# Kernel optimization log

Hardware: AMD Instinct MI355X
Metric: run time of the kernel (lower is better)

The kernel has to match this reference:

```python
import jax, jax.numpy as jnp
import numpy as np

E, H, F, N, B = 512, 8, 2048, 1024, 4
HD = E // H


def setup_inputs() -> dict:
    key = jax.random.key(0)
    ks = jax.random.split(key, 20)
    s = 0.02
    return {
        "node_inputs": jax.random.normal(ks[0], (N, B, E), jnp.float32),
        "parent_mask": jax.random.uniform(ks[1], (B, N, N), jnp.float32),
        "hidden": jax.random.bernoulli(ks[2], 0.5, (B, N, N)),
        "pad_mask": jax.random.bernoulli(ks[3], 0.1, (B, N)),
        "Wp": jax.random.normal(ks[4], (H, E), jnp.float32) * s,
        "bp": jnp.zeros((H,), jnp.float32),
        "Wc": jax.random.normal(ks[5], (H, E), jnp.float32) * s,
        "bc": jnp.zeros((H,), jnp.float32),
        "Wqkv": jax.random.normal(ks[6], (3 * E, E), jnp.float32) * s,
        "bqkv": jnp.zeros((3 * E,), jnp.float32),
        "Wo": jax.random.normal(ks[7], (E, E), jnp.float32) * s,
        "bo": jnp.zeros((E,), jnp.float32),
        "W1": jax.random.normal(ks[8], (F, E), jnp.float32) * s,
        "b1": jnp.zeros((F,), jnp.float32),
        "W2": jax.random.normal(ks[9], (E, F), jnp.float32) * s,
        "b2": jnp.zeros((E,), jnp.float32),
        "ln1_g": jnp.ones((E,), jnp.float32),
        "ln1_b": jnp.zeros((E,), jnp.float32),
        "ln2_g": jnp.ones((E,), jnp.float32),
        "ln2_b": jnp.zeros((E,), jnp.float32),
    }


def _layer_norm(x, g, b, eps=1e-5):
    m = jnp.mean(x, axis=-1, keepdims=True)
    v = jnp.mean((x - m) ** 2, axis=-1, keepdims=True)
    return (x - m) * jax.lax.rsqrt(v + eps) * g + b


def reference(node_inputs, parent_mask, hidden, pad_mask, Wp, bp, Wc, bc,
              Wqkv, bqkv, Wo, bo, W1, b1, W2, b2, ln1_g, ln1_b, ln2_g, ln2_b):
    x = node_inputs  # (N, B, E), seq-first like nn.TransformerEncoderLayer
    # parent/child per-head biases: Linear(E->H), permuted to (B, H, N)
    pbias = jnp.transpose(x @ Wp.T + bp, (1, 2, 0))
    cbias = jnp.transpose(x @ Wc.T + bc, (1, 2, 0))
    # additive attention bias (B, H, N, N)
    am = (jnp.swapaxes(parent_mask, 1, 2)[:, None] * pbias[..., None]
          + parent_mask[:, None] * cbias[..., None])
    am = jnp.where(hidden[:, None], -jnp.inf, am)
    # multi-head self-attention
    qkv = x @ Wqkv.T + bqkv  # (N, B, 3E)
    q, k, v = jnp.split(qkv, 3, axis=-1)

    def heads(t):  # (N, B, E) -> (B, H, N, HD)
        return jnp.transpose(t.reshape(N, B, H, HD), (1, 2, 0, 3))

    q, k, v = heads(q), heads(k), heads(v)
    scores = jnp.einsum("bhqd,bhkd->bhqk", q, k) / jnp.sqrt(jnp.float32(HD)) + am
    scores = jnp.where(pad_mask[:, None, None, :], -jnp.inf, scores)
    attn = jax.nn.softmax(scores, axis=-1)
    ctx = jnp.einsum("bhqk,bhkd->bhqd", attn, v)  # (B, H, N, HD)
    ctx = jnp.transpose(ctx, (2, 0, 1, 3)).reshape(N, B, E)
    attn_out = ctx @ Wo.T + bo
    # post-norm transformer encoder layer (dropout=0, relu activation)
    y = _layer_norm(x + attn_out, ln1_g, ln1_b)
    ff = jax.nn.relu(y @ W1.T + b1) @ W2.T + b2
    return _layer_norm(y + ff, ln2_g, ln2_b)
```

## Files before the change

### kernel.cpp

```cpp
#include <hip/hip_runtime.h>
#include <hip/hip_bf16.h>
#include <stdint.h>

using bf16 = __hip_bfloat16;

typedef __bf16 bf16x8 __attribute__((ext_vector_type(8)));
typedef float  f32x4  __attribute__((ext_vector_type(4)));

__device__ __forceinline__ float bflo(uint32_t u) { return __uint_as_float(u << 16); }
__device__ __forceinline__ float bfhi(uint32_t u) { return __uint_as_float(u & 0xffff0000u); }

__device__ __forceinline__ void load8(const bf16* p, float* f) {
  uint4 u = *(const uint4*)p;
  f[0] = bflo(u.x); f[1] = bfhi(u.x);
  f[2] = bflo(u.y); f[3] = bfhi(u.y);
  f[4] = bflo(u.z); f[5] = bfhi(u.z);
  f[6] = bflo(u.w); f[7] = bfhi(u.w);
}
__device__ __forceinline__ void load8(const float* p, float* f) {
  float4 a = *(const float4*)p, b = *(const float4*)(p + 4);
  f[0] = a.x; f[1] = a.y; f[2] = a.z; f[3] = a.w;
  f[4] = b.x; f[5] = b.y; f[6] = b.z; f[7] = b.w;
}
__device__ __forceinline__ void store1(float* o, float v) { *o = v; }
__device__ __forceinline__ void store1(bf16* o, float v) { *o = __float2bfloat16(v); }
__device__ __forceinline__ uint32_t bfbits(float x) {
  bf16 v = __float2bfloat16(x);
  return (uint32_t)*(uint16_t*)&v;
}

typedef const uint32_t __attribute__((address_space(1)))* gp_t;
typedef uint32_t __attribute__((address_space(3)))* lp_t;
__device__ __forceinline__ void gload16(const void* g, void* l) {
  __builtin_amdgcn_global_load_lds((gp_t)g, (lp_t)l, 16, 0, 0);
}

__global__ __launch_bounds__(256)
void prep_mask(const float* __restrict__ pm, const int* __restrict__ hid,
               const int* __restrict__ padm, uint32_t* __restrict__ mout,
               const float* __restrict__ x, const float* __restrict__ Wqkv,
               const float* __restrict__ Wo, const float* __restrict__ W1,
               const float* __restrict__ W2, bf16* __restrict__ xb,
               bf16* __restrict__ wq, bf16* __restrict__ wob,
               bf16* __restrict__ w1b, bf16* __restrict__ w2b,
               const float* __restrict__ bqkv, const float* __restrict__ bp,
               const float* __restrict__ bc, const float* __restrict__ Wp,
               const float* __restrict__ Wc, float* __restrict__ bias_ext)
{
  __shared__ ushort tileT[128][70];
  const int t = threadIdx.x;
  if (blockIdx.x < 512) {
    const int mb = blockIdx.x;
    const int k0 = (mb & 7) * 128, q0 = ((mb >> 3) & 15) * 64, b = mb >> 7;
    const size_t pb = (size_t)b << 20;
#pragma unroll
    for (int i = 0; i < 8; ++i) {
      int idx = t + i * 256;
      int r = idx >> 4, c4 = (idx & 15) * 4;
      float4 v = *(const float4*)(pm + pb + (size_t)(k0 + r) * 1024 + q0 + c4);
      tileT[r][c4 + 0] = (ushort)bfbits(v.x);
      tileT[r][c4 + 1] = (ushort)bfbits(v.y);
      tileT[r][c4 + 2] = (ushort)bfbits(v.z);
      tileT[r][c4 + 3] = (ushort)bfbits(v.w);
    }
    __syncthreads();
#pragma unroll
    for (int i = 0; i < 8; ++i) {
      int idx = t + i * 256;
      int q = idx >> 5, k4 = (idx & 31) * 4;
      size_t src = pb + (size_t)(q0 + q) * 1024 + k0 + k4;
      int4  hv = *(const int4*)(hid + src);
      float4 pv = *(const float4*)(pm + src);
      int4  pd = *(const int4*)(padm + b * 1024 + k0 + k4);
      uint4 o;
      o.x = (hv.x | pd.x) ? 0xFFFFFFFFu : (((uint32_t)tileT[k4 + 0][q] << 16) | bfbits(pv.x));
      o.y = (hv.y | pd.y) ? 0xFFFFFFFFu : (((uint32_t)tileT[k4 + 1][q] << 16) | bfbits(pv.y));
      o.z = (hv.z | pd.z) ? 0xFFFFFFFFu : (((uint32_t)tileT[k4 + 2][q] << 16) | bfbits(pv.z));
      o.w = (hv.w | pd.w) ? 0xFFFFFFFFu : (((uint32_t)tileT[k4 + 3][q] << 16) | bfbits(pv.w));
      *(uint4*)(mout + src) = o;
    }
    return;
  }
  const int blk = blockIdx.x - 512;
  if (blk < 2560) {
    size_t j = ((size_t)blk * 256 + t) * 8;
    const float* s; bf16* o; size_t off;
    if      (j < 2097152) { s = x;    o = xb;  off = j; }
    else if (j < 2883584) { s = Wqkv; o = wq;  off = j - 2097152; }
    else if (j < 3145728) { s = Wo;   o = wob; off = j - 2883584; }
    else if (j < 4194304) { s = W1;   o = w1b; off = j - 3145728; }
    else                  { s = W2;   o = w2b; off = j - 4194304; }
    float f[8];
    load8(s + off, f);
    uint4 u;
    u.x = (bfbits(f[1]) << 16) | bfbits(f[0]);
    u.y = (bfbits(f[3]) << 16) | bfbits(f[2]);
    u.z = (bfbits(f[5]) << 16) | bfbits(f[4]);
    u.w = (bfbits(f[7]) << 16) | bfbits(f[6]);
    *(uint4*)(o + off) = u;
  } else {
    int sb = blk - 2560;
    if (sb < 2) {
      int j = (sb * 256 + t) * 8;
      if (j < 4096) {
        float f[8]; load8(Wp + j, f);
#pragma unroll
        for (int i = 0; i < 8; ++i) wq[(size_t)1536 * 512 + j + i] = __float2bfloat16(f[i]);
      }
    } else if (sb < 4) {
      int j = ((sb - 2) * 256 + t) * 8;
      if (j < 4096) {
        float f[8]; load8(Wc + j, f);
#pragma unroll
        for (int i = 0; i < 8; ++i) wq[(size_t)1544 * 512 + j + i] = __float2bfloat16(f[i]);
      }
    } else {
      int j = t * 8;
#pragma unroll
      for (int i = 0; i < 8; ++i) {
        int cc = j + i;
        if (cc < 1664) {
          float v = 0.f;
          if (cc < 1536) v = bqkv[cc];
          else if (cc < 1544) v = bp[cc - 1536];
          else if (cc < 1552) v = bc[cc - 1544];
          bias_ext[cc] = v;
        }
      }
    }
  }
}

__global__ __launch_bounds__(256)
void qkv_gemm(const bf16* __restrict__ A, const bf16* __restrict__ W,
              const float* __restrict__ bias, bf16* __restrict__ outb,
              float* __restrict__ outf)
{
  __shared__ bf16 As[2][128 * 64];
  __shared__ bf16 Bs[2][128 * 64];
  const int t = threadIdx.x;
  const int lane = t & 63, wave = t >> 6;
  const int m0 = (blockIdx.x / 13) * 128, n0 = (blockIdx.x % 13) * 128;
  const int wr = wave >> 1, wc = wave & 1;
  const int frow = lane & 15, ksel = (lane >> 4) * 8;
  f32x4 acc[16] = {};
  const bf16* Ab = A + (size_t)m0 * 512;
  const bf16* Wb = W + (size_t)n0 * 512;

  const int ibs = wave * 64 + lane;
#define STAGE(buf, k0)                                                        \
  {                                                                           \
    _Pragma("unroll")                                                         \
    for (int i = 0; i < 4; ++i) {                                             \
      int idx = i * 256 + ibs;                                                \
      gload16(Ab + (size_t)(idx >> 3) * 512 + (k0) + (idx & 7) * 8,           \
              &As[buf][(i * 256 + wave * 64) * 8]);                           \
    }                                                                         \
    _Pragma("unroll")                                                         \
    for (int i = 0; i < 4; ++i) {                                             \
      int idx = i * 256 + ibs;                                                \
      gload16(Wb + (size_t)(idx >> 3) * 512 + (k0) + (idx & 7) * 8,           \
              &Bs[buf][(i * 256 + wave * 64) * 8]);                           \
    }                                                                         \
  }

  STAGE(0, 0);
  __syncthreads();
#pragma unroll
  for (int ks = 0; ks < 8; ++ks) {
    const int cur = ks & 1;
    if (ks < 7) STAGE(cur ^ 1, (ks + 1) * 64);
#pragma unroll
    for (int kk = 0; kk < 64; kk += 32) {
      bf16x8 af[4], bf_[4];
#pragma unroll
      for (int mt = 0; mt < 4; ++mt)
        af[mt] = *(const bf16x8*)(&As[cur][(wr * 64 + mt * 16 + frow) * 64 + kk + ksel]);
#pragma unroll
      for (int nt = 0; nt < 4; ++nt)
        bf_[nt] = *(const bf16x8*)(&Bs[cur][(wc * 64 + nt * 16 + frow) * 64 + kk + ksel]);
#pragma unroll
      for (int mt = 0; mt < 4; ++mt)
#pragma unroll
        for (int nt = 0; nt < 4; ++nt)
          acc[mt * 4 + nt] = __builtin_amdgcn_mfma_f32_16x16x32_bf16(
              af[mt], bf_[nt], acc[mt * 4 + nt], 0, 0, 0);
    }
    __syncthreads();
  }
#undef STAGE

  const int rb = (lane >> 4) * 4, cb = lane & 15;
#pragma unroll
  for (int mt = 0; mt < 4; ++mt)
#pragma unroll
    for (int nt = 0; nt < 4; ++nt) {
      f32x4 a = acc[mt * 4 + nt];
#pragma unroll
      for (int r = 0; r < 4; ++r) {
        int row = m0 + wr * 64 + mt * 16 + rb + r;
        int col = n0 + wc * 64 + nt * 16 + cb;
        if (col >= 1552) continue;
        float v = a[r] + bias[col];
        int n = row >> 2, b = row & 3;
        if (col >= 1536) {
          int j = col - 1536;
          int hh = j & 7;
          outf[(j < 8 ? 0 : 32768) + (b * 8 + hh) * 1024 + n] = v;
        } else {
          int which = col >> 9, hh = (col >> 6) & 7, d = col & 63;
          if (which == 0) v *= 0.125f;
          size_t idx;
          if (which == 2)
            idx = (((size_t)(64 + b * 8 + hh)) << 16) + (size_t)d * 1024 + n;
          else
            idx = (((size_t)(which * 32 + b * 8 + hh)) << 16) + (size_t)n * 64 + d;
          outb[idx] = __float2bfloat16(v);
        }
      }
    }
}

template<int MODE, int BN>
__global__ __launch_bounds__(256)
void gemm_bt(const bf16* __restrict__ A, const bf16* __restrict__ W,
             const float* __restrict__ bias, bf16* __restrict__ outb,
             float* __restrict__ outf, int M, int Nout, int K, int kLen)
{
  constexpr int NT = BN / 32;
  __shared__ bf16 As[128 * 64];
  __shared__ bf16 Bs[BN * 64];
  const int t = threadIdx.x, lane = t & 63, wave = t >> 6;
  const int m0 = blockIdx.y * 128, n0 = blockIdx.x * BN;
  const int kOff = blockIdx.z * kLen;
  if (MODE == 3) outf += (size_t)blockIdx.z * M * Nout;
  const int wr = wave >> 1, wc = wave & 1;
  const int frow = lane & 15, ksel = (lane >> 4) * 8;
  f32x4 acc[4 * NT] = {};
  const bf16* Ab = A + (size_t)m0 * K;
  const bf16* Wb = W + (size_t)n0 * K;

  for (int k0 = kOff; k0 < kOff + kLen; k0 += 64) {
    __syncthreads();
#pragma unroll
    for (int i = 0; i < 4; ++i) {
      int ib = i * 256 + wave * 64;
      int idx = ib + lane;
      gload16(Ab + (size_t)(idx >> 3) * K + k0 + (idx & 7) * 8, As + ib * 8);
    }
#pragma unroll
    for (int i = 0; i < BN / 32; ++i) {
      int ib = i * 256 + wave * 64;
      int idx = ib + lane;
      gload16(Wb + (size_t)(idx >> 3) * K + k0 + (idx & 7) * 8, Bs + ib * 8);
    }
    __syncthreads();
#pragma unroll
    for (int kk = 0; kk < 64; kk += 32) {
      bf16x8 af[4], bf_[NT];
#pragma unroll
      for (int mt = 0; mt < 4; ++mt)
        af[mt] = *(const bf16x8*)(As + (wr * 64 + mt * 16 + frow) * 64 + kk + ksel);
#pragma unroll
      for (int nt = 0; nt < NT; ++nt)
        bf_[nt] = *(const bf16x8*)(Bs + (wc * (BN / 2) + nt * 16 + frow) * 64 + kk + ksel);
#pragma unroll
      for (int mt = 0; mt < 4; ++mt)
#pragma unroll
        for (int nt = 0; nt < NT; ++nt)
          acc[mt * NT + nt] = __builtin_amdgcn_mfma_f32_16x16x32_bf16(
              af[mt], bf_[nt], acc[mt * NT + nt], 0, 0, 0);
    }
  }
  const int rb = (lane >> 4) * 4, cb = lane & 15;
#pragma unroll
  for (int mt = 0; mt < 4; ++mt)
#pragma unroll
    for (int nt = 0; nt < NT; ++nt) {
      f32x4 a = acc[mt * NT + nt];
#pragma unroll
      for (int r = 0; r < 4; ++r) {
        int row = m0 + wr * 64 + mt * 16 + rb + r;
        int col = n0 + wc * (BN / 2) + nt * 16 + cb;
        if (MODE == 3) {
          outf[(size_t)row * Nout + col] = a[r];
        } else {
          float v = a[r] + bias[col];
          if (MODE == 1) v = fmaxf(v, 0.f);
          outb[(size_t)row * Nout + col] = __float2bfloat16(v);
        }
      }
    }
}

__global__ __launch_bounds__(256, 2)
void attn_mfma(const bf16* __restrict__ qkv, const float* __restrict__ pbw,
               const float* __restrict__ cbw, const uint32_t* __restrict__ mpk,
               bf16* __restrict__ ctxo)
{
  __shared__ bf16 Kt[128 * 64];
  __shared__ bf16 Vt[64 * 128];
  __shared__ bf16 Ps[4][16][136];
  const int t = threadIdx.x, lane = t & 63, wave = t >> 6;
  const int g = lane >> 4, c = lane & 15;
  const int h = blockIdx.y, b = blockIdx.z;
  const int q0 = blockIdx.x * 64 + wave * 16;
  const size_t bh = (size_t)b * 8 + h;
  const bf16* Qp = qkv + (bh << 16);
  const bf16* Kp = qkv + ((32 + bh) << 16);
  const bf16* Vg = qkv + ((64 + bh) << 16);

  bf16x8 qa0 = *(const bf16x8*)(Qp + (size_t)(q0 + c) * 64 + g * 8);
  bf16x8 qa1 = *(const bf16x8*)(Qp + (size_t)(q0 + c) * 64 + 32 + g * 8);

  const float pbq = pbw[bh * 1024 + q0 + c];
  const float cbq = cbw[bh * 1024 + q0 + c];
  const uint32_t* mrp = mpk + (((size_t)b * 1024 + q0 + c) << 10);

  f32x4 oacc[4] = {{0,0,0,0},{0,0,0,0},{0,0,0,0},{0,0,0,0}};
  float m = -1e30f, l = 0.f;

  for (int kt = 0; kt < 8; ++kt) {
    const int k0 = kt * 128;
    __syncthreads();
#pragma unroll
    for (int i = 0; i < 4; ++i) {
      int ib = i * 256 + wave * 64;
      int idx = ib + lane;
      int r = idx >> 3, p = idx & 7;
      gload16(Kp + (size_t)(k0 + r) * 64 + ((p ^ (r & 7)) * 8), Kt + ib * 8);
    }
#pragma unroll
    for (int i = 0; i < 4; ++i) {
      int ib = i * 256 + wave * 64;
      int idx = ib + lane;
      int d = idx >> 4, p = idx & 15;
      gload16(Vg + (size_t)d * 1024 + k0 + ((p ^ (d & 15)) * 8), Vt + ib * 8);
    }
    uint4 mu[8];
#pragma unroll
    for (int nt = 0; nt < 8; ++nt)
      mu[nt] = *(const uint4*)(mrp + k0 + nt * 16 + 4 * g);
    __syncthreads();
    f32x4 sacc[8];
#pragma unroll
    for (int nt = 0; nt < 8; ++nt) {
      f32x4 z = {0.f,0.f,0.f,0.f};
      int r = nt * 16 + c;
      bf16x8 k0f = *(const bf16x8*)(Kt + r * 64 + (( g      ^ (c & 7)) * 8));
      bf16x8 k1f = *(const bf16x8*)(Kt + r * 64 + (((4 + g) ^ (c & 7)) * 8));
      z = __builtin_amdgcn_mfma_f32_16x16x32_bf16(k0f, qa0, z, 0, 0, 0);
      z = __builtin_amdgcn_mfma_f32_16x16x32_bf16(k1f, qa1, z, 0, 0, 0);
      sacc[nt] = z;
    }
    float mx = -1e30f;
#pragma unroll
    for (int nt = 0; nt < 8; ++nt) {
      uint32_t uu[4] = {mu[nt].x, mu[nt].y, mu[nt].z, mu[nt].w};
#pragma unroll
      for (int r = 0; r < 4; ++r) {
        float s = sacc[nt][r] + bfhi(uu[r]) * pbq + bflo(uu[r]) * cbq;
        s = (uu[r] == 0xFFFFFFFFu) ? -1e30f : s;
        sacc[nt][r] = s;
        mx = fmaxf(mx, s);
      }
    }
    mx = fmaxf(mx, __shfl_xor(mx, 16));
    mx = fmaxf(mx, __shfl_xor(mx, 32));
    const float newm = fmaxf(m, mx);
    const float al = __expf(m - newm);
    float ps = 0.f;
#pragma unroll
    for (int nt = 0; nt < 8; ++nt) {
      float p0 = (sacc[nt][0] <= -1e29f) ? 0.f : __expf(sacc[nt][0] - newm);
      float p1 = (sacc[nt][1] <= -1e29f) ? 0.f : __expf(sacc[nt][1] - newm);
      float p2 = (sacc[nt][2] <= -1e29f) ? 0.f : __expf(sacc[nt][2] - newm);
      float p3 = (sacc[nt][3] <= -1e29f) ? 0.f : __expf(sacc[nt][3] - newm);
      ps += (p0 + p1) + (p2 + p3);
      uint2 w;
      w.x = (bfbits(p1) << 16) | bfbits(p0);
      w.y = (bfbits(p3) << 16) | bfbits(p2);
      *(uint2*)&Ps[wave][c][nt * 16 + 4 * g] = w;
    }
    ps += __shfl_xor(ps, 16);
    ps += __shfl_xor(ps, 32);
    l = l * al + ps;
    m = newm;
#pragma unroll
    for (int dt = 0; dt < 4; ++dt) {
      oacc[dt][0] *= al; oacc[dt][1] *= al;
      oacc[dt][2] *= al; oacc[dt][3] *= al;
    }
#pragma unroll
    for (int dt = 0; dt < 4; ++dt) {
      int row = dt * 16 + c;
#pragma unroll
      for (int kc = 0; kc < 4; ++kc) {
        bf16x8 vf = *(const bf16x8*)(Vt + row * 128 + (((kc * 4 + g) ^ c) * 8));
        bf16x8 pf = *(const bf16x8*)&Ps[wave][c][kc * 32 + g * 8];
        oacc[dt] = __builtin_amdgcn_mfma_f32_16x16x32_bf16(vf, pf, oacc[dt], 0, 0, 0);
      }
    }
  }
  const int qg = q0 + c;
  const float inv = (l > 0.f) ? 1.f / l : 0.f;
  bf16* out = ctxo + ((size_t)qg * 4 + b) * 512 + h * 64;
#pragma unroll
  for (int dt = 0; dt < 4; ++dt) {
    uint2 w;
    w.x = (bfbits(oacc[dt][1] * inv) << 16) | bfbits(oacc[dt][0] * inv);
    w.y = (bfbits(oacc[dt][3] * inv) << 16) | bfbits(oacc[dt][2] * inv);
    *(uint2*)(out + dt * 16 + 4 * g) = w;
  }
}

template<typename TA, typename TO>
__global__ __launch_bounds__(256)
void ln_res2(const TA* __restrict__ a, const float* __restrict__ p0,
             const float* __restrict__ p1, const float* __restrict__ bias,
             const float* __restrict__ g, const float* __restrict__ be,
             TO* __restrict__ out)
{
  const int wave = threadIdx.x >> 6, lane = threadIdx.x & 63;
  const int m = blockIdx.x * 4 + wave;
  const size_t base = (size_t)m * 512 + lane * 8;
  float va[8], f0[8], f1[8], bb[8];
  load8(a + base, va);
  load8(p0 + base, f0);
  load8(p1 + base, f1);
  load8(bias + lane * 8, bb);
  float v[8], s = 0.f;
#pragma unroll
  for (int j = 0; j < 8; ++j) { v[j] = va[j] + f0[j] + f1[j] + bb[j]; s += v[j]; }
#pragma unroll
  for (int off = 32; off; off >>= 1) s += __shfl_xor(s, off);
  const float mean = s * (1.f / 512.f);
  float q = 0.f;
#pragma unroll
  for (int j = 0; j < 8; ++j) { float d = v[j] - mean; q += d * d; }
#pragma unroll
  for (int off = 32; off; off >>= 1) q += __shfl_xor(q, off);
  const float rs = rsqrtf(q * (1.f / 512.f) + 1e-5f);
  float gv[8], bv[8];
  load8(g + lane * 8, gv);
  load8(be + lane * 8, bv);
#pragma unroll
  for (int j = 0; j < 8; ++j)
    store1(out + base + j, (v[j] - mean) * rs * gv[j] + bv[j]);
}

extern "C" void kernel_launch(void* const* d_in, const int* in_sizes, int n_in,
                              void* d_out, int out_size, void* d_ws, size_t ws_size,
                              hipStream_t stream)
{
  (void)in_sizes; (void)n_in; (void)out_size; (void)ws_size;
  const float* x    = (const float*)d_in[0];
  const float* pm   = (const float*)d_in[1];
  const int*   hid  = (const int*)d_in[2];
  const int*   padm = (const int*)d_in[3];
  const float* Wp   = (const float*)d_in[4];
  const float* bp   = (const float*)d_in[5];
  const float* Wc   = (const float*)d_in[6];
  const float* bc   = (const float*)d_in[7];
  const float* Wqkv = (const float*)d_in[8];
  const float* bqkv = (const float*)d_in[9];
  const float* Wo   = (const float*)d_in[10];
  const float* bo   = (const float*)d_in[11];
  const float* W1   = (const float*)d_in[12];
  const float* b1   = (const float*)d_in[13];
  const float* W2   = (const float*)d_in[14];
  const float* b2   = (const float*)d_in[15];
  const float* g1   = (const float*)d_in[16];
  const float* be1  = (const float*)d_in[17];
  const float* g2   = (const float*)d_in[18];
  const float* be2  = (const float*)d_in[19];

  char* ws = (char*)d_ws;
  bf16*     qkvb  = (bf16*)    (ws);
  float*    pbo   = (float*)   (ws + 12582912);
  float*    cbo   = (float*)   (ws + 12713984);
  uint32_t* mpk   = (uint32_t*)(ws + 12845056);
  bf16*     ctx   = (bf16*)    (ws + 29622272);
  float*    part  = (float*)   (ws);
  bf16*     ff1   = (bf16*)    (ws + 16777216);
  bf16*     y     = (bf16*)    (ws + 33816576);
  bf16*     xb    = (bf16*)    (ws + 38010880);
  bf16*     wqkvb = (bf16*)    (ws + 42205184);
  bf16*     wob   = (bf16*)    (ws + 43909120);
  bf16*     w1b   = (bf16*)    (ws + 44433408);
  bf16*     w2b   = (bf16*)    (ws + 46530560);
  float*    bext  = (float*)   (ws + 48627712);
  float*    part1 = part + (size_t)4096 * 512;

  prep_mask<<<3077, 256, 0, stream>>>(pm, hid, padm, mpk,
                                      x, Wqkv, Wo, W1, W2, xb, wqkvb, wob, w1b, w2b,
                                      bqkv, bp, bc, Wp, Wc, bext);
  qkv_gemm<<<416, 256, 0, stream>>>(xb, wqkvb, bext, qkvb, pbo);
  attn_mfma<<<dim3(16, 8, 4), 256, 0, stream>>>(qkvb, pbo, cbo, mpk, ctx);
  gemm_bt<3, 64><<<dim3(8, 32, 2), 256, 0, stream>>>(ctx, wob, nullptr, nullptr, part, 4096, 512, 512, 256);
  ln_res2<float, bf16><<<1024, 256, 0, stream>>>(x, part, part1, bo, g1, be1, y);
  gemm_bt<1, 128><<<dim3(16, 32), 256, 0, stream>>>(y, w1b, b1, ff1, nullptr, 4096, 2048, 512, 512);
  gemm_bt<3, 64><<<dim3(8, 32, 2), 256, 0, stream>>>(ff1, w2b, nullptr, nullptr, part, 4096, 512, 2048, 1024);
  ln_res2<bf16, float><<<1024, 256, 0, stream>>>(y, part, part1, b2, g2, be2, (float*)d_out);
}
```

Before: 251.2 us.

## Fuse all stages into a persistent cooperative megakernel with grid syncs

Replaces the eight separate kernel launches with one cooperative persistent kernel that loops over task indices per stage and separates stages with grid-wide syncs, falling back to separate launches if cooperative launch is unavailable. The QKV GEMM also loses its double-buffered LDS staging and becomes single-buffered so the stage fits the shared smem layout. The aim is to remove launch overhead and inter-kernel gaps. In exchange, every stage runs at the megakernel's single occupancy and LDS footprint (50 KB, 2 blocks per CU), grid syncs add their own cost, and the QKV GEMM loses its load/compute overlap.

```diff
diff --git a/kernel.cpp b/kernel.cpp
--- a/kernel.cpp
+++ b/kernel.cpp
@@ -1,6 +1,9 @@
 #include <hip/hip_runtime.h>
+#include <hip/hip_cooperative_groups.h>
 #include <hip/hip_bf16.h>
 #include <stdint.h>
+
+namespace cg = cooperative_groups;
 
 using bf16 = __hip_bfloat16;
 
@@ -35,29 +38,31 @@
   __builtin_amdgcn_global_load_lds((gp_t)g, (lp_t)l, 16, 0, 0);
 }
 
-__global__ __launch_bounds__(256)
-void prep_mask(const float* __restrict__ pm, const int* __restrict__ hid,
-               const int* __restrict__ padm, uint32_t* __restrict__ mout,
-               const float* __restrict__ x, const float* __restrict__ Wqkv,
-               const float* __restrict__ Wo, const float* __restrict__ W1,
-               const float* __restrict__ W2, bf16* __restrict__ xb,
-               bf16* __restrict__ wq, bf16* __restrict__ wob,
-               bf16* __restrict__ w1b, bf16* __restrict__ w2b,
-               const float* __restrict__ bqkv, const float* __restrict__ bp,
-               const float* __restrict__ bc, const float* __restrict__ Wp,
-               const float* __restrict__ Wc, float* __restrict__ bias_ext)
-{
-  __shared__ ushort tileT[128][70];
-  const int t = threadIdx.x;
-  if (blockIdx.x < 512) {
-    const int mb = blockIdx.x;
+struct MArgs {
+  const float* x; const float* pm; const int* hid; const int* padm;
+  const float* Wp; const float* bp; const float* Wc; const float* bc;
+  const float* Wqkv; const float* bqkv; const float* Wo; const float* bo;
+  const float* W1; const float* b1; const float* W2; const float* b2;
+  const float* g1; const float* be1; const float* g2; const float* be2;
+  float* d_out;
+  bf16* qkvb; float* pbo; float* cbo; uint32_t* mpk; bf16* ctx;
+  float* part; float* part1; bf16* ff1; bf16* y; bf16* xb; bf16* wqkvb;
+  bf16* wob; bf16* w1b; bf16* w2b; float* bext;
+};
+
+
+__device__ void prep_task(char* smem, int task, int t, const MArgs& A)
+{
+  if (task < 512) {
+    ushort (*tileT)[70] = (ushort(*)[70])smem;
+    const int mb = task;
     const int k0 = (mb & 7) * 128, q0 = ((mb >> 3) & 15) * 64, b = mb >> 7;
     const size_t pb = (size_t)b << 20;
 #pragma unroll
     for (int i = 0; i < 8; ++i) {
       int idx = t + i * 256;
       int r = idx >> 4, c4 = (idx & 15) * 4;
-      float4 v = *(const float4*)(pm + pb + (size_t)(k0 + r) * 1024 + q0 + c4);
+      float4 v = *(const float4*)(A.pm + pb + (size_t)(k0 + r) * 1024 + q0 + c4);
       tileT[r][c4 + 0] = (ushort)bfbits(v.x);
       tileT[r][c4 + 1] = (ushort)bfbits(v.y);
       tileT[r][c4 + 2] = (ushort)bfbits(v.z);
@@ -69,27 +74,28 @@
       int idx = t + i * 256;
       int q = idx >> 5, k4 = (idx & 31) * 4;
       size_t src = pb + (size_t)(q0 + q) * 1024 + k0 + k4;
-      int4  hv = *(const int4*)(hid + src);
-      float4 pv = *(const float4*)(pm + src);
-      int4  pd = *(const int4*)(padm + b * 1024 + k0 + k4);
+      int4  hv = *(const int4*)(A.hid + src);
+      float4 pv = *(const float4*)(A.pm + src);
+      int4  pd = *(const int4*)(A.padm + b * 1024 + k0 + k4);
       uint4 o;
       o.x = (hv.x | pd.x) ? 0xFFFFFFFFu : (((uint32_t)tileT[k4 + 0][q] << 16) | bfbits(pv.x));
       o.y = (hv.y | pd.y) ? 0xFFFFFFFFu : (((uint32_t)tileT[k4 + 1][q] << 16) | bfbits(pv.y));
       o.z = (hv.z | pd.z) ? 0xFFFFFFFFu : (((uint32_t)tileT[k4 + 2][q] << 16) | bfbits(pv.z));
       o.w = (hv.w | pd.w) ? 0xFFFFFFFFu : (((uint32_t)tileT[k4 + 3][q] << 16) | bfbits(pv.w));
-      *(uint4*)(mout + src) = o;
-    }
+      *(uint4*)(A.mpk + src) = o;
+    }
+    __syncthreads();
     return;
   }
-  const int blk = blockIdx.x - 512;
+  const int blk = task - 512;
   if (blk < 2560) {
     size_t j = ((size_t)blk * 256 + t) * 8;
     const float* s; bf16* o; size_t off;
-    if      (j < 2097152) { s = x;    o = xb;  off = j; }
-    else if (j < 2883584) { s = Wqkv; o = wq;  off = j - 2097152; }
-    else if (j < 3145728) { s = Wo;   o = wob; off = j - 2883584; }
-    else if (j < 4194304) { s = W1;   o = w1b; off = j - 3145728; }
-    else                  { s = W2;   o = w2b; off = j - 4194304; }
+    if      (j < 2097152) { s = A.x;    o = A.xb;    off = j; }
+    else if (j < 2883584) { s = A.Wqkv; o = A.wqkvb; off = j - 2097152; }
+    else if (j < 3145728) { s = A.Wo;   o = A.wob;   off = j - 2883584; }
+    else if (j < 4194304) { s = A.W1;   o = A.w1b;   off = j - 3145728; }
+    else                  { s = A.W2;   o = A.w2b;   off = j - 4194304; }
     float f[8];
     load8(s + off, f);
     uint4 u;
@@ -103,16 +109,16 @@
     if (sb < 2) {
       int j = (sb * 256 + t) * 8;
       if (j < 4096) {
-        float f[8]; load8(Wp + j, f);
-#pragma unroll
-        for (int i = 0; i < 8; ++i) wq[(size_t)1536 * 512 + j + i] = __float2bfloat16(f[i]);
+        float f[8]; load8(A.Wp + j, f);
+#pragma unroll
+        for (int i = 0; i < 8; ++i) A.wqkvb[(size_t)1536 * 512 + j + i] = __float2bfloat16(f[i]);
       }
     } else if (sb < 4) {
       int j = ((sb - 2) * 256 + t) * 8;
       if (j < 4096) {
-        float f[8]; load8(Wc + j, f);
-#pragma unroll
-        for (int i = 0; i < 8; ++i) wq[(size_t)1544 * 512 + j + i] = __float2bfloat16(f[i]);
+        float f[8]; load8(A.Wc + j, f);
+#pragma unroll
+        for (int i = 0; i < 8; ++i) A.wqkvb[(size_t)1544 * 512 + j + i] = __float2bfloat16(f[i]);
       }
     } else {
       int j = t * 8;
@@ -121,64 +127,51 @@
         int cc = j + i;
         if (cc < 1664) {
           float v = 0.f;
-          if (cc < 1536) v = bqkv[cc];
-          else if (cc < 1544) v = bp[cc - 1536];
-          else if (cc < 1552) v = bc[cc - 1544];
-          bias_ext[cc] = v;
+          if (cc < 1536) v = A.bqkv[cc];
+          else if (cc < 1544) v = A.bp[cc - 1536];
+          else if (cc < 1552) v = A.bc[cc - 1544];
+          A.bext[cc] = v;
         }
       }
     }
   }
 }
 
-__global__ __launch_bounds__(256)
-void qkv_gemm(const bf16* __restrict__ A, const bf16* __restrict__ W,
-              const float* __restrict__ bias, bf16* __restrict__ outb,
-              float* __restrict__ outf)
-{
-  __shared__ bf16 As[2][128 * 64];
-  __shared__ bf16 Bs[2][128 * 64];
-  const int t = threadIdx.x;
+__device__ void qkv_task(char* smem, int task, int t, const MArgs& A)
+{
+  bf16* As = (bf16*)smem;
+  bf16* Bs = (bf16*)(smem + 16384);
   const int lane = t & 63, wave = t >> 6;
-  const int m0 = (blockIdx.x / 13) * 128, n0 = (blockIdx.x % 13) * 128;
+  const int m0 = (task / 13) * 128, n0 = (task % 13) * 128;
   const int wr = wave >> 1, wc = wave & 1;
   const int frow = lane & 15, ksel = (lane >> 4) * 8;
   f32x4 acc[16] = {};
-  const bf16* Ab = A + (size_t)m0 * 512;
-  const bf16* Wb = W + (size_t)n0 * 512;
-
-  const int ibs = wave * 64 + lane;
-#define STAGE(buf, k0)                                                        \
-  {                                                                           \
-    _Pragma("unroll")                                                         \
-    for (int i = 0; i < 4; ++i) {                                             \
-      int idx = i * 256 + ibs;                                                \
-      gload16(Ab + (size_t)(idx >> 3) * 512 + (k0) + (idx & 7) * 8,           \
-              &As[buf][(i * 256 + wave * 64) * 8]);                           \
-    }                                                                         \
-    _Pragma("unroll")                                                         \
-    for (int i = 0; i < 4; ++i) {                                             \
-      int idx = i * 256 + ibs;                                                \
-      gload16(Wb + (size_t)(idx >> 3) * 512 + (k0) + (idx & 7) * 8,           \
-              &Bs[buf][(i * 256 + wave * 64) * 8]);                           \
-    }                                                                         \
-  }
-
-  STAGE(0, 0);
-  __syncthreads();
-#pragma unroll
-  for (int ks = 0; ks < 8; ++ks) {
-    const int cur = ks & 1;
-    if (ks < 7) STAGE(cur ^ 1, (ks + 1) * 64);
+  const bf16* Ab = A.xb + (size_t)m0 * 512;
+  const bf16* Wb = A.wqkvb + (size_t)n0 * 512;
+  for (int k0 = 0; k0 < 512; k0 += 64) {
+    __syncthreads();
+#pragma unroll
+    for (int i = 0; i < 4; ++i) {
+      int ib = i * 256 + wave * 64;
+      int idx = ib + lane;
+      gload16(Ab + (size_t)(idx >> 3) * 512 + k0 + (idx & 7) * 8, As + ib * 8);
+    }
+#pragma unroll
+    for (int i = 0; i < 4; ++i) {
+      int ib = i * 256 + wave * 64;
+      int idx = ib + lane;
+      gload16(Wb + (size_t)(idx >> 3) * 512 + k0 + (idx & 7) * 8, Bs + ib * 8);
+    }
+    __syncthreads();
 #pragma unroll
     for (int kk = 0; kk < 64; kk += 32) {
       bf16x8 af[4], bf_[4];
 #pragma unroll
       for (int mt = 0; mt < 4; ++mt)
-        af[mt] = *(const bf16x8*)(&As[cur][(wr * 64 + mt * 16 + frow) * 64 + kk + ksel]);
+        af[mt] = *(const bf16x8*)(As + (wr * 64 + mt * 16 + frow) * 64 + kk + ksel);
 #pragma unroll
       for (int nt = 0; nt < 4; ++nt)
-        bf_[nt] = *(const bf16x8*)(&Bs[cur][(wc * 64 + nt * 16 + frow) * 64 + kk + ksel]);
+        bf_[nt] = *(const bf16x8*)(Bs + (wc * 64 + nt * 16 + frow) * 64 + kk + ksel);
 #pragma unroll
       for (int mt = 0; mt < 4; ++mt)
 #pragma unroll
@@ -186,10 +179,7 @@
           acc[mt * 4 + nt] = __builtin_amdgcn_mfma_f32_16x16x32_bf16(
               af[mt], bf_[nt], acc[mt * 4 + nt], 0, 0, 0);
     }
-    __syncthreads();
-  }
-#undef STAGE
-
+  }
   const int rb = (lane >> 4) * 4, cb = lane & 15;
 #pragma unroll
   for (int mt = 0; mt < 4; ++mt)
@@ -201,12 +191,12 @@
         int row = m0 + wr * 64 + mt * 16 + rb + r;
         int col = n0 + wc * 64 + nt * 16 + cb;
         if (col >= 1552) continue;
-        float v = a[r] + bias[col];
+        float v = a[r] + A.bext[col];
         int n = row >> 2, b = row & 3;
         if (col >= 1536) {
           int j = col - 1536;
           int hh = j & 7;
-          outf[(j < 8 ? 0 : 32768) + (b * 8 + hh) * 1024 + n] = v;
+          A.pbo[(j < 8 ? 0 : 32768) + (b * 8 + hh) * 1024 + n] = v;
         } else {
           int which = col >> 9, hh = (col >> 6) & 7, d = col & 63;
           if (which == 0) v *= 0.125f;
@@ -215,30 +205,149 @@
             idx = (((size_t)(64 + b * 8 + hh)) << 16) + (size_t)d * 1024 + n;
           else
             idx = (((size_t)(which * 32 + b * 8 + hh)) << 16) + (size_t)n * 64 + d;
-          outb[idx] = __float2bfloat16(v);
+          A.qkvb[idx] = __float2bfloat16(v);
         }
       }
     }
 }
 
+__device__ void attn_task(char* smem, int task, int t, const MArgs& A)
+{
+  bf16* Kt = (bf16*)smem;
+  bf16* Vt = (bf16*)(smem + 16384);
+  bf16 (*Ps)[16][136] = (bf16(*)[16][136])(smem + 32768);
+  const int lane = t & 63, wave = t >> 6;
+  const int g = lane >> 4, c = lane & 15;
+  const int bx = task & 15, h = (task >> 4) & 7, b = task >> 7;
+  const int q0 = bx * 64 + wave * 16;
+  const size_t bh = (size_t)b * 8 + h;
+  const bf16* Qp = A.qkvb + (bh << 16);
+  const bf16* Kp = A.qkvb + ((32 + bh) << 16);
+  const bf16* Vg = A.qkvb + ((64 + bh) << 16);
+
+  bf16x8 qa0 = *(const bf16x8*)(Qp + (size_t)(q0 + c) * 64 + g * 8);
+  bf16x8 qa1 = *(const bf16x8*)(Qp + (size_t)(q0 + c) * 64 + 32 + g * 8);
+
+  const float pbq = A.pbo[bh * 1024 + q0 + c];
+  const float cbq = A.cbo[bh * 1024 + q0 + c];
+  const uint32_t* mrp = A.mpk + (((size_t)b * 1024 + q0 + c) << 10);
+
+  f32x4 oacc[4] = {{0,0,0,0},{0,0,0,0},{0,0,0,0},{0,0,0,0}};
+  float m = -1e30f, l = 0.f;
+
+  for (int kt = 0; kt < 8; ++kt) {
+    const int k0 = kt * 128;
+    __syncthreads();
+#pragma unroll
+    for (int i = 0; i < 4; ++i) {
+      int ib = i * 256 + wave * 64;
+      int idx = ib + lane;
+      int r = idx >> 3, p = idx & 7;
+      gload16(Kp + (size_t)(k0 + r) * 64 + ((p ^ (r & 7)) * 8), Kt + ib * 8);
+    }
+#pragma unroll
+    for (int i = 0; i < 4; ++i) {
+      int ib = i * 256 + wave * 64;
+      int idx = ib + lane;
+      int d = idx >> 4, p = idx & 15;
+      gload16(Vg + (size_t)d * 1024 + k0 + ((p ^ (d & 15)) * 8), Vt + ib * 8);
+    }
+    uint4 mu[8];
+#pragma unroll
+    for (int nt = 0; nt < 8; ++nt)
+      mu[nt] = *(const uint4*)(mrp + k0 + nt * 16 + 4 * g);
+    __syncthreads();
+    f32x4 sacc[8];
+#pragma unroll
+    for (int nt = 0; nt < 8; ++nt) {
+      f32x4 z = {0.f,0.f,0.f,0.f};
+      int r = nt * 16 + c;
+      bf16x8 k0f = *(const bf16x8*)(Kt + r * 64 + (( g      ^ (c & 7)) * 8));
+      bf16x8 k1f = *(const bf16x8*)(Kt + r * 64 + (((4 + g) ^ (c & 7)) * 8));
+      z = __builtin_amdgcn_mfma_f32_16x16x32_bf16(k0f, qa0, z, 0, 0, 0);
+      z = __builtin_amdgcn_mfma_f32_16x16x32_bf16(k1f, qa1, z, 0, 0, 0);
+      sacc[nt] = z;
+    }
+    float mx = -1e30f;
+#pragma unroll
+    for (int nt = 0; nt < 8; ++nt) {
+      uint32_t uu[4] = {mu[nt].x, mu[nt].y, mu[nt].z, mu[nt].w};
+#pragma unroll
+      for (int r = 0; r < 4; ++r) {
+        float s = sacc[nt][r] + bfhi(uu[r]) * pbq + bflo(uu[r]) * cbq;
+        s = (uu[r] == 0xFFFFFFFFu) ? -1e30f : s;
+        sacc[nt][r] = s;
+        mx = fmaxf(mx, s);
+      }
+    }
+    mx = fmaxf(mx, __shfl_xor(mx, 16));
+    mx = fmaxf(mx, __shfl_xor(mx, 32));
+    const float newm = fmaxf(m, mx);
+    const float al = __expf(m - newm);
+    float ps = 0.f;
+#pragma unroll
+    for (int nt = 0; nt < 8; ++nt) {
+      float p0 = (sacc[nt][0] <= -1e29f) ? 0.f : __expf(sacc[nt][0] - newm);
+      float p1 = (sacc[nt][1] <= -1e29f) ? 0.f : __expf(sacc[nt][1] - newm);
+      float p2 = (sacc[nt][2] <= -1e29f) ? 0.f : __expf(sacc[nt][2] - newm);
+      float p3 = (sacc[nt][3] <= -1e29f) ? 0.f : __expf(sacc[nt][3] - newm);
+      ps += (p0 + p1) + (p2 + p3);
+      uint2 w;
+      w.x = (bfbits(p1) << 16) | bfbits(p0);
+      w.y = (bfbits(p3) << 16) | bfbits(p2);
+      *(uint2*)&Ps[wave][c][nt * 16 + 4 * g] = w;
+    }
+    ps += __shfl_xor(ps, 16);
+    ps += __shfl_xor(ps, 32);
+    l = l * al + ps;
+    m = newm;
+#pragma unroll
+    for (int dt = 0; dt < 4; ++dt) {
+      oacc[dt][0] *= al; oacc[dt][1] *= al;
+      oacc[dt][2] *= al; oacc[dt][3] *= al;
+    }
+#pragma unroll
+    for (int dt = 0; dt < 4; ++dt) {
+      int row = dt * 16 + c;
+#pragma unroll
+      for (int kc = 0; kc < 4; ++kc) {
+        bf16x8 vf = *(const bf16x8*)(Vt + row * 128 + (((kc * 4 + g) ^ c) * 8));
+        bf16x8 pf = *(const bf16x8*)&Ps[wave][c][kc * 32 + g * 8];
+        oacc[dt] = __builtin_amdgcn_mfma_f32_16x16x32_bf16(vf, pf, oacc[dt], 0, 0, 0);
+      }
+    }
+  }
+  __syncthreads();
+  const int qg = q0 + c;
+  const float inv = (l > 0.f) ? 1.f / l : 0.f;
+  bf16* out = A.ctx + ((size_t)qg * 4 + b) * 512 + h * 64;
+#pragma unroll
+  for (int dt = 0; dt < 4; ++dt) {
+    uint2 w;
+    w.x = (bfbits(oacc[dt][1] * inv) << 16) | bfbits(oacc[dt][0] * inv);
+    w.y = (bfbits(oacc[dt][3] * inv) << 16) | bfbits(oacc[dt][2] * inv);
+    *(uint2*)(out + dt * 16 + 4 * g) = w;
+  }
+}
+
 template<int MODE, int BN>
-__global__ __launch_bounds__(256)
-void gemm_bt(const bf16* __restrict__ A, const bf16* __restrict__ W,
-             const float* __restrict__ bias, bf16* __restrict__ outb,
-             float* __restrict__ outf, int M, int Nout, int K, int kLen)
+__device__ void gemm_task(char* smem, int bx, int by, int bz, int t,
+                          const bf16* __restrict__ Ag, const bf16* __restrict__ Wg,
+                          const float* __restrict__ bias, bf16* __restrict__ outb,
+                          float* __restrict__ outf, int M, int Nout, int K, int kLen)
 {
   constexpr int NT = BN / 32;
-  __shared__ bf16 As[128 * 64];
-  __shared__ bf16 Bs[BN * 64];
-  const int t = threadIdx.x, lane = t & 63, wave = t >> 6;
-  const int m0 = blockIdx.y * 128, n0 = blockIdx.x * BN;
-  const int kOff = blockIdx.z * kLen;
-  if (MODE == 3) outf += (size_t)blockIdx.z * M * Nout;
+  bf16* As = (bf16*)smem;
+  bf16* Bs = (bf16*)(smem + 16384);
+  const int lane = t & 63, wave = t >> 6;
+  const int m0 = by * 128, n0 = bx * BN;
+  const int kOff = bz * kLen;
+  if (MODE == 3) outf += (size_t)bz * M * Nout;
   const int wr = wave >> 1, wc = wave & 1;
   const int frow = lane & 15, ksel = (lane >> 4) * 8;
   f32x4 acc[4 * NT] = {};
-  const bf16* Ab = A + (size_t)m0 * K;
-  const bf16* Wb = W + (size_t)n0 * K;
+  const bf16* Ab = Ag + (size_t)m0 * K;
+  const bf16* Wb = Wg + (size_t)n0 * K;
 
   for (int k0 = kOff; k0 < kOff + kLen; k0 += 64) {
     __syncthreads();
@@ -293,136 +402,15 @@
     }
 }
 
-__global__ __launch_bounds__(256, 2)
-void attn_mfma(const bf16* __restrict__ qkv, const float* __restrict__ pbw,
-               const float* __restrict__ cbw, const uint32_t* __restrict__ mpk,
-               bf16* __restrict__ ctxo)
-{
-  __shared__ bf16 Kt[128 * 64];
-  __shared__ bf16 Vt[64 * 128];
-  __shared__ bf16 Ps[4][16][136];
-  const int t = threadIdx.x, lane = t & 63, wave = t >> 6;
-  const int g = lane >> 4, c = lane & 15;
-  const int h = blockIdx.y, b = blockIdx.z;
-  const int q0 = blockIdx.x * 64 + wave * 16;
-  const size_t bh = (size_t)b * 8 + h;
-  const bf16* Qp = qkv + (bh << 16);
-  const bf16* Kp = qkv + ((32 + bh) << 16);
-  const bf16* Vg = qkv + ((64 + bh) << 16);
-
-  bf16x8 qa0 = *(const bf16x8*)(Qp + (size_t)(q0 + c) * 64 + g * 8);
-  bf16x8 qa1 = *(const bf16x8*)(Qp + (size_t)(q0 + c) * 64 + 32 + g * 8);
-
-  const float pbq = pbw[bh * 1024 + q0 + c];
-  const float cbq = cbw[bh * 1024 + q0 + c];
-  const uint32_t* mrp = mpk + (((size_t)b * 1024 + q0 + c) << 10);
-
-  f32x4 oacc[4] = {{0,0,0,0},{0,0,0,0},{0,0,0,0},{0,0,0,0}};
-  float m = -1e30f, l = 0.f;
-
-  for (int kt = 0; kt < 8; ++kt) {
-    const int k0 = kt * 128;
-    __syncthreads();
-#pragma unroll
-    for (int i = 0; i < 4; ++i) {
-      int ib = i * 256 + wave * 64;
-      int idx = ib + lane;
-      int r = idx >> 3, p = idx & 7;
-      gload16(Kp + (size_t)(k0 + r) * 64 + ((p ^ (r & 7)) * 8), Kt + ib * 8);
-    }
-#pragma unroll
-    for (int i = 0; i < 4; ++i) {
-      int ib = i * 256 + wave * 64;
-      int idx = ib + lane;
-      int d = idx >> 4, p = idx & 15;
-      gload16(Vg + (size_t)d * 1024 + k0 + ((p ^ (d & 15)) * 8), Vt + ib * 8);
-    }
-    uint4 mu[8];
-#pragma unroll
-    for (int nt = 0; nt < 8; ++nt)
-      mu[nt] = *(const uint4*)(mrp + k0 + nt * 16 + 4 * g);
-    __syncthreads();
-    f32x4 sacc[8];
-#pragma unroll
-    for (int nt = 0; nt < 8; ++nt) {
-      f32x4 z = {0.f,0.f,0.f,0.f};
-      int r = nt * 16 + c;
-      bf16x8 k0f = *(const bf16x8*)(Kt + r * 64 + (( g      ^ (c & 7)) * 8));
-      bf16x8 k1f = *(const bf16x8*)(Kt + r * 64 + (((4 + g) ^ (c & 7)) * 8));
-      z = __builtin_amdgcn_mfma_f32_16x16x32_bf16(k0f, qa0, z, 0, 0, 0);
-      z = __builtin_amdgcn_mfma_f32_16x16x32_bf16(k1f, qa1, z, 0, 0, 0);
-      sacc[nt] = z;
-    }
-    float mx = -1e30f;
-#pragma unroll
-    for (int nt = 0; nt < 8; ++nt) {
-      uint32_t uu[4] = {mu[nt].x, mu[nt].y, mu[nt].z, mu[nt].w};
-#pragma unroll
-      for (int r = 0; r < 4; ++r) {
-        float s = sacc[nt][r] + bfhi(uu[r]) * pbq + bflo(uu[r]) * cbq;
-        s = (uu[r] == 0xFFFFFFFFu) ? -1e30f : s;
-        sacc[nt][r] = s;
-        mx = fmaxf(mx, s);
-      }
-    }
-    mx = fmaxf(mx, __shfl_xor(mx, 16));
-    mx = fmaxf(mx, __shfl_xor(mx, 32));
-    const float newm = fmaxf(m, mx);
-    const float al = __expf(m - newm);
-    float ps = 0.f;
-#pragma unroll
-    for (int nt = 0; nt < 8; ++nt) {
-      float p0 = (sacc[nt][0] <= -1e29f) ? 0.f : __expf(sacc[nt][0] - newm);
-      float p1 = (sacc[nt][1] <= -1e29f) ? 0.f : __expf(sacc[nt][1] - newm);
-      float p2 = (sacc[nt][2] <= -1e29f) ? 0.f : __expf(sacc[nt][2] - newm);
-      float p3 = (sacc[nt][3] <= -1e29f) ? 0.f : __expf(sacc[nt][3] - newm);
-      ps += (p0 + p1) + (p2 + p3);
-      uint2 w;
-      w.x = (bfbits(p1) << 16) | bfbits(p0);
-      w.y = (bfbits(p3) << 16) | bfbits(p2);
-      *(uint2*)&Ps[wave][c][nt * 16 + 4 * g] = w;
-    }
-    ps += __shfl_xor(ps, 16);
-    ps += __shfl_xor(ps, 32);
-    l = l * al + ps;
-    m = newm;
-#pragma unroll
-    for (int dt = 0; dt < 4; ++dt) {
-      oacc[dt][0] *= al; oacc[dt][1] *= al;
-      oacc[dt][2] *= al; oacc[dt][3] *= al;
-    }
-#pragma unroll
-    for (int dt = 0; dt < 4; ++dt) {
-      int row = dt * 16 + c;
-#pragma unroll
-      for (int kc = 0; kc < 4; ++kc) {
-        bf16x8 vf = *(const bf16x8*)(Vt + row * 128 + (((kc * 4 + g) ^ c) * 8));
-        bf16x8 pf = *(const bf16x8*)&Ps[wave][c][kc * 32 + g * 8];
-        oacc[dt] = __builtin_amdgcn_mfma_f32_16x16x32_bf16(vf, pf, oacc[dt], 0, 0, 0);
-      }
-    }
-  }
-  const int qg = q0 + c;
-  const float inv = (l > 0.f) ? 1.f / l : 0.f;
-  bf16* out = ctxo + ((size_t)qg * 4 + b) * 512 + h * 64;
-#pragma unroll
-  for (int dt = 0; dt < 4; ++dt) {
-    uint2 w;
-    w.x = (bfbits(oacc[dt][1] * inv) << 16) | bfbits(oacc[dt][0] * inv);
-    w.y = (bfbits(oacc[dt][3] * inv) << 16) | bfbits(oacc[dt][2] * inv);
-    *(uint2*)(out + dt * 16 + 4 * g) = w;
-  }
-}
-
 template<typename TA, typename TO>
-__global__ __launch_bounds__(256)
-void ln_res2(const TA* __restrict__ a, const float* __restrict__ p0,
-             const float* __restrict__ p1, const float* __restrict__ bias,
-             const float* __restrict__ g, const float* __restrict__ be,
-             TO* __restrict__ out)
-{
-  const int wave = threadIdx.x >> 6, lane = threadIdx.x & 63;
-  const int m = blockIdx.x * 4 + wave;
+__device__ void ln_task(int task, int t,
+                        const TA* __restrict__ a, const float* __restrict__ p0,
+                        const float* __restrict__ p1, const float* __restrict__ bias,
+                        const float* __restrict__ g, const float* __restrict__ be,
+                        TO* __restrict__ out)
+{
+  const int wave = t >> 6, lane = t & 63;
+  const int m = task * 4 + wave;
   const size_t base = (size_t)m * 512 + lane * 8;
   float va[8], f0[8], f1[8], bb[8];
   load8(a + base, va);
@@ -449,57 +437,147 @@
     store1(out + base + j, (v[j] - mean) * rs * gv[j] + bv[j]);
 }
 
+__global__ __launch_bounds__(256, 2)
+void mega(MArgs A)
+{
+  __shared__ __align__(16) char smem[50176];
+  cg::grid_group grid = cg::this_grid();
+  const int t = threadIdx.x;
+  const int nb = gridDim.x;
+
+  for (int task = blockIdx.x; task < 3077; task += nb) prep_task(smem, task, t, A);
+  grid.sync();
+  for (int task = blockIdx.x; task < 416; task += nb) qkv_task(smem, task, t, A);
+  grid.sync();
+  for (int task = blockIdx.x; task < 512; task += nb) attn_task(smem, task, t, A);
+  grid.sync();
+  for (int task = blockIdx.x; task < 512; task += nb)
+    gemm_task<3, 64>(smem, task & 7, (task >> 3) & 31, task >> 8, t,
+                     A.ctx, A.wob, nullptr, nullptr, A.part, 4096, 512, 512, 256);
+  grid.sync();
+  for (int task = blockIdx.x; task < 1024; task += nb)
+    ln_task<float, bf16>(task, t, A.x, A.part, A.part1, A.bo, A.g1, A.be1, A.y);
+  grid.sync();
+  for (int task = blockIdx.x; task < 512; task += nb)
+    gemm_task<1, 128>(smem, task & 15, task >> 4, 0, t,
+                      A.y, A.w1b, A.b1, A.ff1, nullptr, 4096, 2048, 512, 512);
+  grid.sync();
+  for (int task = blockIdx.x; task < 512; task += nb)
+    gemm_task<3, 64>(smem, task & 7, (task >> 3) & 31, task >> 8, t,
+                     A.ff1, A.w2b, nullptr, nullptr, A.part, 4096, 512, 2048, 1024);
+  grid.sync();
+  for (int task = blockIdx.x; task < 1024; task += nb)
+    ln_task<bf16, float>(task, t, A.y, A.part, A.part1, A.b2, A.g2, A.be2, A.d_out);
+}
+
+__global__ __launch_bounds__(256) void k_prep(MArgs A) {
+  __shared__ __align__(16) char smem[17920];
+  prep_task(smem, blockIdx.x, threadIdx.x, A);
+}
+__global__ __launch_bounds__(256) void k_qkv(MArgs A) {
+  __shared__ __align__(16) char smem[32768];
+  qkv_task(smem, blockIdx.x, threadIdx.x, A);
+}
+__global__ __launch_bounds__(256, 2) void k_attn(MArgs A) {
+  __shared__ __align__(16) char smem[50176];
+  attn_task(smem, blockIdx.x, threadIdx.x, A);
+}
+__global__ __launch_bounds__(256) void k_wo(MArgs A) {
+  __shared__ __align__(16) char smem[24576];
+  int task = blockIdx.x;
+  gemm_task<3, 64>(smem, task & 7, (task >> 3) & 31, task >> 8, threadIdx.x,
+                   A.ctx, A.wob, nullptr, nullptr, A.part, 4096, 512, 512, 256);
+}
+__global__ __launch_bounds__(256) void k_ln1(MArgs A) {
+  ln_task<float, bf16>(blockIdx.x, threadIdx.x, A.x, A.part, A.part1, A.bo, A.g1, A.be1, A.y);
+}
+__global__ __launch_bounds__(256) void k_ff1(MArgs A) {
+  __shared__ __align__(16) char smem[32768];
+  int task = blockIdx.x;
+  gemm_task<1, 128>(smem, task & 15, task >> 4, 0, threadIdx.x,
+                    A.y, A.w1b, A.b1, A.ff1, nullptr, 4096, 2048, 512, 512);
+}
+__global__ __launch_bounds__(256) void k_ff2(MArgs A) {
+  __shared__ __align__(16) char smem[24576];
+  int task = blockIdx.x;
+  gemm_task<3, 64>(smem, task & 7, (task >> 3) & 31, task >> 8, threadIdx.x,
+                   A.ff1, A.w2b, nullptr, nullptr, A.part, 4096, 512, 2048, 1024);
+}
+__global__ __launch_bounds__(256) void k_ln2(MArgs A) {
+  ln_task<bf16, float>(blockIdx.x, threadIdx.x, A.y, A.part, A.part1, A.b2, A.g2, A.be2, A.d_out);
+}
+
 extern "C" void kernel_launch(void* const* d_in, const int* in_sizes, int n_in,
                               void* d_out, int out_size, void* d_ws, size_t ws_size,
                               hipStream_t stream)
 {
   (void)in_sizes; (void)n_in; (void)out_size; (void)ws_size;
-  const float* x    = (const float*)d_in[0];
-  const float* pm   = (const float*)d_in[1];
-  const int*   hid  = (const int*)d_in[2];
-  const int*   padm = (const int*)d_in[3];
-  const float* Wp   = (const float*)d_in[4];
-  const float* bp   = (const float*)d_in[5];
-  const float* Wc   = (const float*)d_in[6];
-  const float* bc   = (const float*)d_in[7];
-  const float* Wqkv = (const float*)d_in[8];
-  const float* bqkv = (const float*)d_in[9];
-  const float* Wo   = (const float*)d_in[10];
-  const float* bo   = (const float*)d_in[11];
-  const float* W1   = (const float*)d_in[12];
-  const float* b1   = (const float*)d_in[13];
-  const float* W2   = (const float*)d_in[14];
-  const float* b2   = (const float*)d_in[15];
-  const float* g1   = (const float*)d_in[16];
-  const float* be1  = (const float*)d_in[17];
-  const float* g2   = (const float*)d_in[18];
-  const float* be2  = (const float*)d_in[19];
-
   char* ws = (char*)d_ws;
-  bf16*     qkvb  = (bf16*)    (ws);
-  float*    pbo   = (float*)   (ws + 12582912);
-  float*    cbo   = (float*)   (ws + 12713984);
-  uint32_t* mpk   = (uint32_t*)(ws + 12845056);
-  bf16*     ctx   = (bf16*)    (ws + 29622272);
-  float*    part  = (float*)   (ws);
-  bf16*     ff1   = (bf16*)    (ws + 16777216);
-  bf16*     y     = (bf16*)    (ws + 33816576);
-  bf16*     xb    = (bf16*)    (ws + 38010880);
-  bf16*     wqkvb = (bf16*)    (ws + 42205184);
-  bf16*     wob   = (bf16*)    (ws + 43909120);
-  bf16*     w1b   = (bf16*)    (ws + 44433408);
-  bf16*     w2b   = (bf16*)    (ws + 46530560);
-  float*    bext  = (float*)   (ws + 48627712);
-  float*    part1 = part + (size_t)4096 * 512;
-
-  prep_mask<<<3077, 256, 0, stream>>>(pm, hid, padm, mpk,
-                                      x, Wqkv, Wo, W1, W2, xb, wqkvb, wob, w1b, w2b,
-                                      bqkv, bp, bc, Wp, Wc, bext);
-  qkv_gemm<<<416, 256, 0, stream>>>(xb, wqkvb, bext, qkvb, pbo);
-  attn_mfma<<<dim3(16, 8, 4), 256, 0, stream>>>(qkvb, pbo, cbo, mpk, ctx);
-  gemm_bt<3, 64><<<dim3(8, 32, 2), 256, 0, stream>>>(ctx, wob, nullptr, nullptr, part, 4096, 512, 512, 256);
-  ln_res2<float, bf16><<<1024, 256, 0, stream>>>(x, part, part1, bo, g1, be1, y);
-  gemm_bt<1, 128><<<dim3(16, 32), 256, 0, stream>>>(y, w1b, b1, ff1, nullptr, 4096, 2048, 512, 512);
-  gemm_bt<3, 64><<<dim3(8, 32, 2), 256, 0, stream>>>(ff1, w2b, nullptr, nullptr, part, 4096, 512, 2048, 1024);
-  ln_res2<bf16, float><<<1024, 256, 0, stream>>>(y, part, part1, b2, g2, be2, (float*)d_out);
-}
+
+  MArgs a;
+  a.x    = (const float*)d_in[0];
+  a.pm   = (const float*)d_in[1];
+  a.hid  = (const int*)d_in[2];
+  a.padm = (const int*)d_in[3];
+  a.Wp   = (const float*)d_in[4];
+  a.bp   = (const float*)d_in[5];
+  a.Wc   = (const float*)d_in[6];
+  a.bc   = (const float*)d_in[7];
+  a.Wqkv = (const float*)d_in[8];
+  a.bqkv = (const float*)d_in[9];
+  a.Wo   = (const float*)d_in[10];
+  a.bo   = (const float*)d_in[11];
+  a.W1   = (const float*)d_in[12];
+  a.b1   = (const float*)d_in[13];
+  a.W2   = (const float*)d_in[14];
+  a.b2   = (const float*)d_in[15];
+  a.g1   = (const float*)d_in[16];
+  a.be1  = (const float*)d_in[17];
+  a.g2   = (const float*)d_in[18];
+  a.be2  = (const float*)d_in[19];
+  a.d_out = (float*)d_out;
+
+  a.qkvb  = (bf16*)    (ws);
+  a.pbo   = (float*)   (ws + 12582912);
+  a.cbo   = (float*)   (ws + 12713984);
+  a.mpk   = (uint32_t*)(ws + 12845056);
+  a.ctx   = (bf16*)    (ws + 29622272);
+  a.part  = (float*)   (ws);
+  a.part1 = a.part + (size_t)4096 * 512;
+  a.ff1   = (bf16*)    (ws + 16777216);
+  a.y     = (bf16*)    (ws + 33816576);
+  a.xb    = (bf16*)    (ws + 38010880);
+  a.wqkvb = (bf16*)    (ws + 42205184);
+  a.wob   = (bf16*)    (ws + 43909120);
+  a.w1b   = (bf16*)    (ws + 44433408);
+  a.w2b   = (bf16*)    (ws + 46530560);
+  a.bext  = (float*)   (ws + 48627712);
+
+  bool coop_ok = false;
+  int coop_attr = 0;
+  if (hipDeviceGetAttribute(&coop_attr, hipDeviceAttributeCooperativeLaunch, 0) == hipSuccess
+      && coop_attr) {
+    int maxb = 0, ncu = 0;
+    if (hipOccupancyMaxActiveBlocksPerMultiprocessor(&maxb, (const void*)mega, 256, 0) == hipSuccess
+        && hipDeviceGetAttribute(&ncu, hipDeviceAttributeMultiprocessorCount, 0) == hipSuccess) {
+      long cap = (long)maxb * (long)ncu;
+      int nblk = (int)(cap < 768 ? cap : 768);
+      if (nblk >= 512) {
+        void* params[] = { (void*)&a };
+        if (hipLaunchCooperativeKernel((const void*)mega, dim3(nblk), dim3(256),
+                                       params, 0, stream) == hipSuccess)
+          coop_ok = true;
+      }
+    }
+  }
+  if (!coop_ok) {
+    k_prep<<<3077, 256, 0, stream>>>(a);
+    k_qkv<<<416, 256, 0, stream>>>(a);
+    k_attn<<<512, 256, 0, stream>>>(a);
+    k_wo<<<512, 256, 0, stream>>>(a);
+    k_ln1<<<1024, 256, 0, stream>>>(a);
+    k_ff1<<<512, 256, 0, stream>>>(a);
+    k_ff2<<<512, 256, 0, stream>>>(a);
+    k_ln2<<<1024, 256, 0, stream>>>(a);
+  }
+}
```

Result: slower. 260.7 us (+3.8%).
